# Kernel optimization log

Measured on AMD Instinct MI355X. Metric: run time of the kernel, lower is better.

## Reference

```python
import jax, jax.numpy as jnp
import numpy as np

V, E, H2, K = 30000, 256, 256, 13  # vocab, embed dim, per-direction hidden, num tags
B, T = 64, 512


def setup_inputs() -> dict:
    key = jax.random.key(0)
    ks = jax.random.split(key, 12)
    s = 0.1
    return {
        "x": jax.random.randint(ks[0], (B, T), 0, V, dtype=jnp.int32),
        "emb": jax.random.normal(ks[1], (V, E), dtype=jnp.float32) * s,
        "w_ih_f": jax.random.normal(ks[2], (4 * H2, E), dtype=jnp.float32) * s,
        "w_hh_f": jax.random.normal(ks[3], (4 * H2, H2), dtype=jnp.float32) * s,
        "b_ih_f": jnp.zeros((4 * H2,), jnp.float32),
        "b_hh_f": jnp.zeros((4 * H2,), jnp.float32),
        "w_ih_b": jax.random.normal(ks[4], (4 * H2, E), dtype=jnp.float32) * s,
        "w_hh_b": jax.random.normal(ks[5], (4 * H2, H2), dtype=jnp.float32) * s,
        "b_ih_b": jnp.zeros((4 * H2,), jnp.float32),
        "b_hh_b": jnp.zeros((4 * H2,), jnp.float32),
        "w_out": jax.random.normal(ks[6], (K, 2 * H2), dtype=jnp.float32) * s,
        "b_out": jnp.zeros((K,), jnp.float32),
        "start_trans": jax.random.normal(ks[7], (K,), dtype=jnp.float32) * s,
        "end_trans": jax.random.normal(ks[8], (K,), dtype=jnp.float32) * s,
        "trans": jax.random.normal(ks[9], (K, K), dtype=jnp.float32) * s,
    }


def _lstm_dir(xg, w_hh, reverse):
    # xg: [T, B, 4H] precomputed input-side gate pre-activations (PyTorch i|f|g|o order)
    Bsz, H = xg.shape[1], w_hh.shape[1]

    def step(carry, g_in):
        h, c = carry
        g = g_in + h @ w_hh.T
        i, f, gg, o = jnp.split(g, 4, axis=-1)
        c = jax.nn.sigmoid(f) * c + jax.nn.sigmoid(i) * jnp.tanh(gg)
        h = jax.nn.sigmoid(o) * jnp.tanh(c)
        return (h, c), h

    init = (jnp.zeros((Bsz, H), xg.dtype), jnp.zeros((Bsz, H), xg.dtype))
    _, hs = jax.lax.scan(step, init, xg, reverse=reverse)
    return hs  # [T, B, H]


def reference(x, emb, w_ih_f, w_hh_f, b_ih_f, b_hh_f, w_ih_b, w_hh_b, b_ih_b, b_hh_b,
              w_out, b_out, start_trans, end_trans, trans):
    e = emb[x].transpose(1, 0, 2)                     # [T, B, E] time-major
    xg_f = e @ w_ih_f.T + (b_ih_f + b_hh_f)           # [T, B, 4H] (fold both biases)
    xg_b = e @ w_ih_b.T + (b_ih_b + b_hh_b)
    h_f = _lstm_dir(xg_f, w_hh_f, reverse=False)
    h_b = _lstm_dir(xg_b, w_hh_b, reverse=True)
    h = jnp.concatenate([h_f, h_b], axis=-1)          # [T, B, 2H]; dropout = identity (eval)
    emissions = h @ w_out.T + b_out                   # [T, B, K]

    # CRF Viterbi decode (torchcrf semantics, full mask)
    score = start_trans + emissions[0]                # [B, K]

    def vstep(score, emit_t):
        s = score[:, :, None] + trans[None] + emit_t[:, None, :]  # [B, K_prev, K_next]
        return s.max(axis=1), s.argmax(axis=1)

    score, bps = jax.lax.scan(vstep, score, emissions[1:])        # bps: [T-1, B, K]
    score = score + end_trans
    best_last = jnp.argmax(score, axis=-1)            # [B]
    best_score = jnp.max(score, axis=-1)              # [B]

    def btstep(tag, bp_t):
        prev = jnp.take_along_axis(bp_t, tag[:, None], axis=1)[:, 0]
        return prev, prev

    _, path_head = jax.lax.scan(btstep, best_last, bps, reverse=True)  # [T-1, B]
    path = jnp.concatenate([path_head, best_last[None]], axis=0).T     # [B, T]
    return path, best_score
```

## Files before the change

### kernel.cpp

```cpp
#include <hip/hip_runtime.h>
#include <stdint.h>
#include <stddef.h>

#define T_LEN  512
#define BATCH  64
#define NTAG   13
#define CT     64
#define NCHUNK 8

__device__ __forceinline__ float sigm(float x) { return 1.0f / (1.0f + expf(-x)); }

__global__ __launch_bounds__(256) void xg_gemm(
    const int* __restrict__ x, const float* __restrict__ emb,
    const float* __restrict__ w_ih_f, const float* __restrict__ w_ih_b,
    const float* __restrict__ b_ih_f, const float* __restrict__ b_hh_f,
    const float* __restrict__ b_ih_b, const float* __restrict__ b_hh_b,
    float* __restrict__ xg_ws, int chunk)
{
    const int tid = threadIdx.x;
    const int mt = blockIdx.x;
    const int nt = blockIdx.y;
    const int d  = blockIdx.z;
    const int tbase = (d == 0 ? chunk : (NCHUNK - 1 - chunk)) * CT;
    const float* W  = (d == 0) ? w_ih_f : w_ih_b;
    const float* bi = (d == 0) ? b_ih_f : b_ih_b;
    const float* bh = (d == 0) ? b_hh_f : b_hh_b;

    __shared__ __align__(16) float Wl[16][132];
    __shared__ __align__(16) float El[16][132];
    __shared__ int tok[128];

    if (tid < 128) {
        int col = nt * 128 + tid;
        tok[tid] = x[(col & 63) * T_LEN + tbase + (col >> 6)];
    }
    __syncthreads();

    const int r  = tid >> 1;
    const int c8 = (tid & 1) * 8;
    const int tm = tid >> 4;
    const int tn = tid & 15;

    float acc[8][8];
#pragma unroll
    for (int i = 0; i < 8; i++)
#pragma unroll
        for (int jz = 0; jz < 8; jz++) acc[i][jz] = 0.0f;

    const float* wrow = &W[(size_t)(mt * 128 + r) * 256];
    const float* erow = &emb[(size_t)tok[r] * 256];

    for (int kb = 0; kb < 256; kb += 16) {
        float4 w0 = *(const float4*)&wrow[kb + c8];
        float4 w1 = *(const float4*)&wrow[kb + c8 + 4];
        float4 e0 = *(const float4*)&erow[kb + c8];
        float4 e1 = *(const float4*)&erow[kb + c8 + 4];
        __syncthreads();
        Wl[c8+0][r] = w0.x; Wl[c8+1][r] = w0.y; Wl[c8+2][r] = w0.z; Wl[c8+3][r] = w0.w;
        Wl[c8+4][r] = w1.x; Wl[c8+5][r] = w1.y; Wl[c8+6][r] = w1.z; Wl[c8+7][r] = w1.w;
        El[c8+0][r] = e0.x; El[c8+1][r] = e0.y; El[c8+2][r] = e0.z; El[c8+3][r] = e0.w;
        El[c8+4][r] = e1.x; El[c8+5][r] = e1.y; El[c8+6][r] = e1.z; El[c8+7][r] = e1.w;
        __syncthreads();
#pragma unroll
        for (int kk = 0; kk < 16; kk++) {
            float a[8], b[8];
            *(float4*)&a[0] = *(const float4*)&Wl[kk][tm*8];
            *(float4*)&a[4] = *(const float4*)&Wl[kk][tm*8+4];
            *(float4*)&b[0] = *(const float4*)&El[kk][tn*8];
            *(float4*)&b[4] = *(const float4*)&El[kk][tn*8+4];
#pragma unroll
            for (int i = 0; i < 8; i++)
#pragma unroll
                for (int jz = 0; jz < 8; jz++)
                    acc[i][jz] += a[i] * b[jz];
        }
    }

    const int colbase = nt * 128 + tn * 8;
    const int j  = colbase >> 6;
    const int b0 = colbase & 63;
#pragma unroll
    for (int gi = 0; gi < 8; gi++) {
        int g = mt * 128 + tm * 8 + gi;
        float bias = bi[g] + bh[g];
        float* dst = &xg_ws[(((size_t)(d * CT + j) * 1024 + g) << 6) + b0];
        float4 v0 = make_float4(acc[gi][0]+bias, acc[gi][1]+bias, acc[gi][2]+bias, acc[gi][3]+bias);
        float4 v1 = make_float4(acc[gi][4]+bias, acc[gi][5]+bias, acc[gi][6]+bias, acc[gi][7]+bias);
        *(float4*)dst       = v0;
        *(float4*)(dst + 4) = v1;
    }
}

__global__ __launch_bounds__(256) void lstm_chunk(
    const float* __restrict__ xg_ws,
    const float* __restrict__ w_hh_f, const float* __restrict__ w_hh_b,
    float* h_ex, float* c_state, float* h_all, int* flags, int chunk)
{
    const int tid = threadIdx.x;
    const int bid = blockIdx.x;
    const int dg    = bid & 7;
    const int slice = bid >> 3;
    const int dir = dg & 1;
    const int grp = dg >> 1;
    const int h_base = slice * 8;
    const int sbase  = grp * 16;

    __shared__ __align__(16) float w_lds[32][260];
    __shared__ __align__(16) float h_lds[16][260];
    __shared__ __align__(16) float red[4][32][20];
    __shared__ float gatebuf[32][17];

    const float* W = dir ? w_hh_b : w_hh_f;
    for (int idx = tid; idx < 32 * 256; idx += 256) {
        int rr = idx >> 8, jj = idx & 255;
        w_lds[rr][jj] = W[(size_t)((rr >> 3) * 256 + h_base + (rr & 7)) * 256 + jj];
    }

    const int s_g  = tid & 15;
    const int ih_g = tid >> 4;
    float c_val = 0.0f;
    if (tid < 128)
        c_val = c_state[(size_t)(dir * 64 + sbase + s_g) * 256 + h_base + ih_g];

    {
        const int s = tid >> 4, tn = tid & 15;
        const float* src = &h_ex[((size_t)dg * 16 + s) * 256];
#pragma unroll
        for (int i = 0; i < 16; i++)
            h_lds[s][tn + 16 * i] =
                __hip_atomic_load(&src[tn + 16 * i], __ATOMIC_RELAXED, __HIP_MEMORY_SCOPE_AGENT);
    }
    __syncthreads();

    const int kc   = tid >> 5;
    const int tile = tid & 31;
    const int gt = tile >> 2;
    const int st = tile & 3;
    const float* wr[4] = { &w_lds[gt][0], &w_lds[8+gt][0], &w_lds[16+gt][0], &w_lds[24+gt][0] };
    const float* hr[4] = { &h_lds[st][0], &h_lds[4+st][0], &h_lds[8+st][0],  &h_lds[12+st][0] };

    float xg0 = 0.f, xg1 = 0.f, xg2 = 0.f, xg3 = 0.f;
    {
        const int jslot0 = dir ? (CT - 1) : 0;
        if (tid < 128) {
            const float* xp = &xg_ws[(((size_t)(dir * CT + jslot0) * 1024) + h_base + ih_g) * 64 + sbase + s_g];
            xg0 = xp[0];
            xg1 = xp[1 * 256 * 64];
            xg2 = xp[2 * 256 * 64];
            xg3 = xp[3 * 256 * 64];
        }
    }

#pragma unroll 1
    for (int tl = 0; tl < CT; tl++) {
        const int jslot = dir ? (CT - 1 - tl) : tl;
        const int t = (dir ? (NCHUNK - 1 - chunk) : chunk) * CT + jslot;
        const int sc = chunk * CT + tl + 1;
        const int par = sc & 1;

        float acc[4][4];
#pragma unroll
        for (int gi = 0; gi < 4; gi++)
#pragma unroll
            for (int si = 0; si < 4; si++) acc[gi][si] = 0.0f;

        const int j0 = kc * 32;
#pragma unroll
        for (int m = 0; m < 8; m++) {
            const int jj = j0 + m * 4;
            float4 w4[4], h4[4];
#pragma unroll
            for (int i = 0; i < 4; i++) w4[i] = *(const float4*)(wr[i] + jj);
#pragma unroll
            for (int i = 0; i < 4; i++) h4[i] = *(const float4*)(hr[i] + jj);
#pragma unroll
            for (int gi = 0; gi < 4; gi++)
#pragma unroll
                for (int si = 0; si < 4; si++)
                    acc[gi][si] += w4[gi].x*h4[si].x + w4[gi].y*h4[si].y
                                 + w4[gi].z*h4[si].z + w4[gi].w*h4[si].w;
        }

        if (kc >= 4) {
#pragma unroll
            for (int gi = 0; gi < 4; gi++)
                *(float4*)&red[kc-4][tile][gi*4] =
                    make_float4(acc[gi][0], acc[gi][1], acc[gi][2], acc[gi][3]);
        }
        __syncthreads();
        if (kc < 4) {
#pragma unroll
            for (int gi = 0; gi < 4; gi++) {
                float4 v = *(const float4*)&red[kc][tile][gi*4];
                acc[gi][0] += v.x; acc[gi][1] += v.y; acc[gi][2] += v.z; acc[gi][3] += v.w;
            }
        }
        __syncthreads();
        if (kc >= 1 && kc < 4) {
#pragma unroll
            for (int gi = 0; gi < 4; gi++)
                *(float4*)&red[kc-1][tile][gi*4] =
                    make_float4(acc[gi][0], acc[gi][1], acc[gi][2], acc[gi][3]);
        }
        __syncthreads();
        if (kc == 0) {
#pragma unroll
            for (int p = 0; p < 3; p++)
#pragma unroll
                for (int gi = 0; gi < 4; gi++) {
                    float4 v = *(const float4*)&red[p][tile][gi*4];
                    acc[gi][0] += v.x; acc[gi][1] += v.y; acc[gi][2] += v.z; acc[gi][3] += v.w;
                }
#pragma unroll
            for (int gi = 0; gi < 4; gi++)
#pragma unroll
                for (int si = 0; si < 4; si++)
                    gatebuf[8*gi + gt][4*si + st] = acc[gi][si];
        }
        __syncthreads();

        float hv = 0.0f;
        if (tid < 128) {
            float gI = gatebuf[ih_g     ][s_g] + xg0;
            float gF = gatebuf[8  + ih_g][s_g] + xg1;
            float gG = gatebuf[16 + ih_g][s_g] + xg2;
            float gO = gatebuf[24 + ih_g][s_g] + xg3;
            c_val = sigm(gF) * c_val + sigm(gI) * tanhf(gG);
            hv = sigm(gO) * tanhf(c_val);
            __hip_atomic_store(&h_ex[(((size_t)par * 8 + dg) * 16 + s_g) * 256 + h_base + ih_g],
                               hv, __ATOMIC_RELAXED, __HIP_MEMORY_SCOPE_AGENT);
        }
        __syncthreads();

        if (tid == 0)
            __hip_atomic_store(&flags[dg * 32 + slice], sc, __ATOMIC_RELAXED, __HIP_MEMORY_SCOPE_AGENT);

        if (tid < 128) {
            h_all[((size_t)t * 64 + sbase + s_g) * 512 + dir * 256 + h_base + ih_g] = hv;
            if (tl + 1 < CT) {
                const int jn = dir ? (jslot - 1) : (jslot + 1);
                const float* xp = &xg_ws[(((size_t)(dir * CT + jn) * 1024) + h_base + ih_g) * 64 + sbase + s_g];
                xg0 = xp[0];
                xg1 = xp[1 * 256 * 64];
                xg2 = xp[2 * 256 * 64];
                xg3 = xp[3 * 256 * 64];
            }
        }

        if (tid < 64) {
            const int* fp = &flags[dg * 32 + (tid & 31)];
            int guard = 0;
            int v = __hip_atomic_load(fp, __ATOMIC_RELAXED, __HIP_MEMORY_SCOPE_AGENT);
            while (__ballot(v < sc) != 0ull) {
                __builtin_amdgcn_s_sleep(4);
                v = __hip_atomic_load(fp, __ATOMIC_RELAXED, __HIP_MEMORY_SCOPE_AGENT);
                if (++guard > (1 << 20)) break;
            }
        }
        __syncthreads();

        {
            const int s = tid >> 4, tn = tid & 15;
            const float* src = &h_ex[(((size_t)par * 8 + dg) * 16 + s) * 256];
#pragma unroll
            for (int i = 0; i < 16; i++)
                h_lds[s][tn + 16 * i] =
                    __hip_atomic_load(&src[tn + 16 * i], __ATOMIC_RELAXED, __HIP_MEMORY_SCOPE_AGENT);
        }
        __syncthreads();
    }

    if (tid < 128)
        c_state[(size_t)(dir * 64 + sbase + s_g) * 256 + h_base + ih_g] = c_val;
}

__global__ __launch_bounds__(256) void emis_kernel(
    const float* __restrict__ h_all, const float* __restrict__ w_out,
    const float* __restrict__ b_out, float* __restrict__ emis)
{
    const int row = blockIdx.x * 16 + (threadIdx.x >> 4);
    const int k   = threadIdx.x & 15;
    const float* hr = &h_all[(size_t)row * 512];
    const float* wr = &w_out[(size_t)(k < NTAG ? k : 0) * 512];
    float acc = 0.0f;
#pragma unroll 8
    for (int e = 0; e < 512; e += 4) {
        float4 h4 = *(const float4*)&hr[e];
        float4 w4 = *(const float4*)&wr[e];
        acc += h4.x*w4.x + h4.y*w4.y + h4.z*w4.z + h4.w*w4.w;
    }
    if (k < NTAG) emis[(size_t)row * NTAG + k] = acc + b_out[k];
}

__global__ __launch_bounds__(64) void viterbi_kernel(
    const float* __restrict__ emis, const float* __restrict__ start_trans,
    const float* __restrict__ end_trans, const float* __restrict__ trans,
    float* __restrict__ out)
{
    const int b = blockIdx.x;
    const int k = threadIdx.x;
    __shared__ float em[T_LEN * NTAG];
    __shared__ unsigned char bp[T_LEN][16];

    for (int t = k; t < T_LEN; t += 64) {
        const float* src = &emis[((size_t)t * 64 + b) * NTAG];
#pragma unroll
        for (int kk = 0; kk < NTAG; kk++)
            em[t * NTAG + kk] = src[kk];
    }
    __syncthreads();

    float tc[NTAG];
#pragma unroll
    for (int kp = 0; kp < NTAG; kp++)
        tc[kp] = (k < NTAG) ? trans[kp * NTAG + k] : 0.0f;

    float score = (k < NTAG) ? (start_trans[k] + em[k]) : -3.0e38f;

    for (int t = 1; t < T_LEN; t++) {
        float best = -3.0e38f;
        int bi = 0;
#pragma unroll
        for (int kp = 0; kp < NTAG; kp++) {
            float v = __shfl(score, kp) + tc[kp];
            if (v > best) { best = v; bi = kp; }
        }
        if (k < NTAG) {
            score = best + em[t * NTAG + k];
            bp[t][k] = (unsigned char)bi;
        }
    }
    if (k < NTAG) score += end_trans[k];
    else score = -3.0e38f;
    __syncthreads();

    float bs = -3.0e38f;
    int tag = 0;
#pragma unroll
    for (int kk = 0; kk < NTAG; kk++) {
        float v = __shfl(score, kk);
        if (v > bs) { bs = v; tag = kk; }
    }
    if (k == 0) {
        out[32768 + b] = bs;
        int tg = tag;
        out[b * T_LEN + (T_LEN - 1)] = (float)tg;
        for (int t = T_LEN - 1; t >= 1; t--) {
            tg = bp[t][tg];
            out[b * T_LEN + t - 1] = (float)tg;
        }
    }
}

extern "C" void kernel_launch(void* const* d_in, const int* in_sizes, int n_in,
                              void* d_out, int out_size, void* d_ws, size_t ws_size,
                              hipStream_t stream)
{
    (void)in_sizes; (void)n_in; (void)out_size; (void)ws_size;
    const int*   x    = (const int*)  d_in[0];
    const float* emb  = (const float*)d_in[1];
    const float* wihf = (const float*)d_in[2];
    const float* whhf = (const float*)d_in[3];
    const float* bihf = (const float*)d_in[4];
    const float* bhhf = (const float*)d_in[5];
    const float* wihb = (const float*)d_in[6];
    const float* whhb = (const float*)d_in[7];
    const float* bihb = (const float*)d_in[8];
    const float* bhhb = (const float*)d_in[9];
    const float* wout = (const float*)d_in[10];
    const float* bout = (const float*)d_in[11];
    const float* stt  = (const float*)d_in[12];
    const float* ent  = (const float*)d_in[13];
    const float* trn  = (const float*)d_in[14];
    float* out = (float*)d_out;

    char* ws = (char*)d_ws;
    size_t off = 0;
    float* xg_ws = (float*)(ws + off); off += (size_t)2 * CT * 1024 * 64 * 4;
    float* h_all = (float*)(ws + off); off += (size_t)T_LEN * 64 * 512 * 4;
    float* h_ex  = (float*)(ws + off); off += (size_t)2 * 8 * 16 * 256 * 4;
    float* c_st  = (float*)(ws + off); off += (size_t)2 * 64 * 256 * 4;
    float* emis  = (float*)(ws + off); off += (size_t)T_LEN * 64 * NTAG * 4;
    int*   flags = (int*)  (ws + off); off += 8 * 32 * 4;

    hipMemsetAsync(h_ex,  0, (size_t)2 * 8 * 16 * 256 * 4, stream);
    hipMemsetAsync(c_st,  0, (size_t)2 * 64 * 256 * 4, stream);
    hipMemsetAsync(flags, 0, 8 * 32 * 4, stream);

    for (int c = 0; c < NCHUNK; c++) {
        xg_gemm<<<dim3(8, 32, 2), 256, 0, stream>>>(x, emb, wihf, wihb,
                                                    bihf, bhhf, bihb, bhhb, xg_ws, c);
        lstm_chunk<<<256, 256, 0, stream>>>(xg_ws, whhf, whhb, h_ex, c_st, h_all, flags, c);
    }
    emis_kernel<<<2048, 256, 0, stream>>>(h_all, wout, bout, emis);
    viterbi_kernel<<<64, 64, 0, stream>>>(emis, stt, ent, trn, out);
}
```

Measured before the change: 3.833 ms.

## Halve LSTM recurrence grid by giving each block 16 hidden units

Each persistent recurrence block now owns 16 hidden units (64 gate rows) instead of 8, so the grid drops from 256 to 128 blocks. All 256 threads take part in the gate nonlinearity, and each group barrier waits on 16 flags instead of 32. The intent is to cut the cost of cross-block synchronisation per timestep and to use otherwise idle threads. In exchange each block does twice the FMA work per step, holds more registers and LDS, and the spin-wait now sleeps only after a few polls.

```diff
diff --git a/kernel.cpp b/kernel.cpp
--- a/kernel.cpp
+++ b/kernel.cpp
@@ -101,26 +101,26 @@
     const int dg    = bid & 7;
     const int slice = bid >> 3;
     const int dir = dg & 1;
-    const int grp = dg >> 1;
-    const int h_base = slice * 8;
-    const int sbase  = grp * 16;
-
-    __shared__ __align__(16) float w_lds[32][260];
+    const int sg  = dg >> 1;
+    const int h_base = slice * 16;
+    const int sbase  = sg * 16;
+
+    __shared__ __align__(16) float w_lds[64][260];
     __shared__ __align__(16) float h_lds[16][260];
-    __shared__ __align__(16) float red[4][32][20];
-    __shared__ float gatebuf[32][17];
+    __shared__ __align__(16) float red[4][32][36];
+    __shared__ float gatebuf[64][17];
 
     const float* W = dir ? w_hh_b : w_hh_f;
-    for (int idx = tid; idx < 32 * 256; idx += 256) {
-        int rr = idx >> 8, jj = idx & 255;
-        w_lds[rr][jj] = W[(size_t)((rr >> 3) * 256 + h_base + (rr & 7)) * 256 + jj];
+    for (int idx = tid; idx < 4096; idx += 256) {
+        int rr = idx >> 6;
+        int c4 = (idx & 63) << 2;
+        int row = (rr >> 4) * 256 + h_base + (rr & 15);
+        *(float4*)&w_lds[rr][c4] = *(const float4*)&W[(size_t)row * 256 + c4];
     }
 
     const int s_g  = tid & 15;
     const int ih_g = tid >> 4;
-    float c_val = 0.0f;
-    if (tid < 128)
-        c_val = c_state[(size_t)(dir * 64 + sbase + s_g) * 256 + h_base + ih_g];
+    float c_val = c_state[(size_t)(dir * 64 + sbase + s_g) * 256 + h_base + ih_g];
 
     {
         const int s = tid >> 4, tn = tid & 15;
@@ -134,21 +134,23 @@
 
     const int kc   = tid >> 5;
     const int tile = tid & 31;
-    const int gt = tile >> 2;
-    const int st = tile & 3;
-    const float* wr[4] = { &w_lds[gt][0], &w_lds[8+gt][0], &w_lds[16+gt][0], &w_lds[24+gt][0] };
-    const float* hr[4] = { &h_lds[st][0], &h_lds[4+st][0], &h_lds[8+st][0],  &h_lds[12+st][0] };
+    const int rowt = tile >> 2;
+    const int st   = tile & 3;
+    const float* wrp[8];
+#pragma unroll
+    for (int i = 0; i < 8; i++) wrp[i] = &w_lds[rowt + i * 8][0];
+    const float* hrp[4];
+#pragma unroll
+    for (int i = 0; i < 4; i++) hrp[i] = &h_lds[st + i * 4][0];
 
     float xg0 = 0.f, xg1 = 0.f, xg2 = 0.f, xg3 = 0.f;
     {
         const int jslot0 = dir ? (CT - 1) : 0;
-        if (tid < 128) {
-            const float* xp = &xg_ws[(((size_t)(dir * CT + jslot0) * 1024) + h_base + ih_g) * 64 + sbase + s_g];
-            xg0 = xp[0];
-            xg1 = xp[1 * 256 * 64];
-            xg2 = xp[2 * 256 * 64];
-            xg3 = xp[3 * 256 * 64];
-        }
+        const float* xp = &xg_ws[(((size_t)(dir * CT + jslot0) * 1024) + h_base + ih_g) * 64 + sbase + s_g];
+        xg0 = xp[0];
+        xg1 = xp[1 * 256 * 64];
+        xg2 = xp[2 * 256 * 64];
+        xg3 = xp[3 * 256 * 64];
     }
 
 #pragma unroll 1
@@ -158,103 +160,98 @@
         const int sc = chunk * CT + tl + 1;
         const int par = sc & 1;
 
-        float acc[4][4];
-#pragma unroll
-        for (int gi = 0; gi < 4; gi++)
-#pragma unroll
-            for (int si = 0; si < 4; si++) acc[gi][si] = 0.0f;
+        float acc[8][4];
+#pragma unroll
+        for (int ri = 0; ri < 8; ri++)
+#pragma unroll
+            for (int si = 0; si < 4; si++) acc[ri][si] = 0.0f;
 
         const int j0 = kc * 32;
 #pragma unroll
         for (int m = 0; m < 8; m++) {
             const int jj = j0 + m * 4;
-            float4 w4[4], h4[4];
-#pragma unroll
-            for (int i = 0; i < 4; i++) w4[i] = *(const float4*)(wr[i] + jj);
-#pragma unroll
-            for (int i = 0; i < 4; i++) h4[i] = *(const float4*)(hr[i] + jj);
-#pragma unroll
-            for (int gi = 0; gi < 4; gi++)
+            float4 h4[4];
+#pragma unroll
+            for (int i = 0; i < 4; i++) h4[i] = *(const float4*)(hrp[i] + jj);
+#pragma unroll
+            for (int ri = 0; ri < 8; ri++) {
+                float4 w4 = *(const float4*)(wrp[ri] + jj);
 #pragma unroll
                 for (int si = 0; si < 4; si++)
-                    acc[gi][si] += w4[gi].x*h4[si].x + w4[gi].y*h4[si].y
-                                 + w4[gi].z*h4[si].z + w4[gi].w*h4[si].w;
+                    acc[ri][si] += w4.x*h4[si].x + w4.y*h4[si].y
+                                 + w4.z*h4[si].z + w4.w*h4[si].w;
+            }
         }
 
         if (kc >= 4) {
 #pragma unroll
-            for (int gi = 0; gi < 4; gi++)
-                *(float4*)&red[kc-4][tile][gi*4] =
-                    make_float4(acc[gi][0], acc[gi][1], acc[gi][2], acc[gi][3]);
+            for (int ri = 0; ri < 8; ri++)
+                *(float4*)&red[kc-4][tile][ri*4] =
+                    make_float4(acc[ri][0], acc[ri][1], acc[ri][2], acc[ri][3]);
         }
         __syncthreads();
         if (kc < 4) {
 #pragma unroll
-            for (int gi = 0; gi < 4; gi++) {
-                float4 v = *(const float4*)&red[kc][tile][gi*4];
-                acc[gi][0] += v.x; acc[gi][1] += v.y; acc[gi][2] += v.z; acc[gi][3] += v.w;
+            for (int ri = 0; ri < 8; ri++) {
+                float4 v = *(const float4*)&red[kc][tile][ri*4];
+                acc[ri][0] += v.x; acc[ri][1] += v.y; acc[ri][2] += v.z; acc[ri][3] += v.w;
             }
         }
         __syncthreads();
         if (kc >= 1 && kc < 4) {
 #pragma unroll
-            for (int gi = 0; gi < 4; gi++)
-                *(float4*)&red[kc-1][tile][gi*4] =
-                    make_float4(acc[gi][0], acc[gi][1], acc[gi][2], acc[gi][3]);
+            for (int ri = 0; ri < 8; ri++)
+                *(float4*)&red[kc-1][tile][ri*4] =
+                    make_float4(acc[ri][0], acc[ri][1], acc[ri][2], acc[ri][3]);
         }
         __syncthreads();
         if (kc == 0) {
 #pragma unroll
             for (int p = 0; p < 3; p++)
 #pragma unroll
-                for (int gi = 0; gi < 4; gi++) {
-                    float4 v = *(const float4*)&red[p][tile][gi*4];
-                    acc[gi][0] += v.x; acc[gi][1] += v.y; acc[gi][2] += v.z; acc[gi][3] += v.w;
+                for (int ri = 0; ri < 8; ri++) {
+                    float4 v = *(const float4*)&red[p][tile][ri*4];
+                    acc[ri][0] += v.x; acc[ri][1] += v.y; acc[ri][2] += v.z; acc[ri][3] += v.w;
                 }
 #pragma unroll
-            for (int gi = 0; gi < 4; gi++)
+            for (int ri = 0; ri < 8; ri++)
 #pragma unroll
                 for (int si = 0; si < 4; si++)
-                    gatebuf[8*gi + gt][4*si + st] = acc[gi][si];
-        }
-        __syncthreads();
-
-        float hv = 0.0f;
-        if (tid < 128) {
-            float gI = gatebuf[ih_g     ][s_g] + xg0;
-            float gF = gatebuf[8  + ih_g][s_g] + xg1;
-            float gG = gatebuf[16 + ih_g][s_g] + xg2;
-            float gO = gatebuf[24 + ih_g][s_g] + xg3;
-            c_val = sigm(gF) * c_val + sigm(gI) * tanhf(gG);
-            hv = sigm(gO) * tanhf(c_val);
-            __hip_atomic_store(&h_ex[(((size_t)par * 8 + dg) * 16 + s_g) * 256 + h_base + ih_g],
-                               hv, __ATOMIC_RELAXED, __HIP_MEMORY_SCOPE_AGENT);
-        }
+                    gatebuf[rowt + ri*8][st + si*4] = acc[ri][si];
+        }
+        __syncthreads();
+
+        float gI = gatebuf[     ih_g][s_g] + xg0;
+        float gF = gatebuf[16 + ih_g][s_g] + xg1;
+        float gG = gatebuf[32 + ih_g][s_g] + xg2;
+        float gO = gatebuf[48 + ih_g][s_g] + xg3;
+        c_val = sigm(gF) * c_val + sigm(gI) * tanhf(gG);
+        float hv = sigm(gO) * tanhf(c_val);
+        __hip_atomic_store(&h_ex[(((size_t)par * 8 + dg) * 16 + s_g) * 256 + h_base + ih_g],
+                           hv, __ATOMIC_RELAXED, __HIP_MEMORY_SCOPE_AGENT);
         __syncthreads();
 
         if (tid == 0)
-            __hip_atomic_store(&flags[dg * 32 + slice], sc, __ATOMIC_RELAXED, __HIP_MEMORY_SCOPE_AGENT);
-
-        if (tid < 128) {
-            h_all[((size_t)t * 64 + sbase + s_g) * 512 + dir * 256 + h_base + ih_g] = hv;
-            if (tl + 1 < CT) {
-                const int jn = dir ? (jslot - 1) : (jslot + 1);
-                const float* xp = &xg_ws[(((size_t)(dir * CT + jn) * 1024) + h_base + ih_g) * 64 + sbase + s_g];
-                xg0 = xp[0];
-                xg1 = xp[1 * 256 * 64];
-                xg2 = xp[2 * 256 * 64];
-                xg3 = xp[3 * 256 * 64];
-            }
+            __hip_atomic_store(&flags[dg * 16 + slice], sc, __ATOMIC_RELAXED, __HIP_MEMORY_SCOPE_AGENT);
+
+        h_all[((size_t)t * 64 + sbase + s_g) * 512 + dir * 256 + h_base + ih_g] = hv;
+        if (tl + 1 < CT) {
+            const int jn = dir ? (jslot - 1) : (jslot + 1);
+            const float* xp = &xg_ws[(((size_t)(dir * CT + jn) * 1024) + h_base + ih_g) * 64 + sbase + s_g];
+            xg0 = xp[0];
+            xg1 = xp[1 * 256 * 64];
+            xg2 = xp[2 * 256 * 64];
+            xg3 = xp[3 * 256 * 64];
         }
 
         if (tid < 64) {
-            const int* fp = &flags[dg * 32 + (tid & 31)];
-            int guard = 0;
+            const int* fp = &flags[dg * 16 + (tid & 15)];
+            int spins = 0;
             int v = __hip_atomic_load(fp, __ATOMIC_RELAXED, __HIP_MEMORY_SCOPE_AGENT);
             while (__ballot(v < sc) != 0ull) {
-                __builtin_amdgcn_s_sleep(4);
+                if (++spins > 4) __builtin_amdgcn_s_sleep(2);
                 v = __hip_atomic_load(fp, __ATOMIC_RELAXED, __HIP_MEMORY_SCOPE_AGENT);
-                if (++guard > (1 << 20)) break;
+                if (spins > (1 << 20)) break;
             }
         }
         __syncthreads();
@@ -270,8 +267,7 @@
         __syncthreads();
     }
 
-    if (tid < 128)
-        c_state[(size_t)(dir * 64 + sbase + s_g) * 256 + h_base + ih_g] = c_val;
+    c_state[(size_t)(dir * 64 + sbase + s_g) * 256 + h_base + ih_g] = c_val;
 }
 
 __global__ __launch_bounds__(256) void emis_kernel(
@@ -381,16 +377,16 @@
     float* h_ex  = (float*)(ws + off); off += (size_t)2 * 8 * 16 * 256 * 4;
     float* c_st  = (float*)(ws + off); off += (size_t)2 * 64 * 256 * 4;
     float* emis  = (float*)(ws + off); off += (size_t)T_LEN * 64 * NTAG * 4;
-    int*   flags = (int*)  (ws + off); off += 8 * 32 * 4;
+    int*   flags = (int*)  (ws + off); off += 8 * 16 * 4;
 
     hipMemsetAsync(h_ex,  0, (size_t)2 * 8 * 16 * 256 * 4, stream);
     hipMemsetAsync(c_st,  0, (size_t)2 * 64 * 256 * 4, stream);
-    hipMemsetAsync(flags, 0, 8 * 32 * 4, stream);
+    hipMemsetAsync(flags, 0, 8 * 16 * 4, stream);
 
     for (int c = 0; c < NCHUNK; c++) {
         xg_gemm<<<dim3(8, 32, 2), 256, 0, stream>>>(x, emb, wihf, wihb,
                                                     bihf, bhhf, bihb, bhhb, xg_ws, c);
-        lstm_chunk<<<256, 256, 0, stream>>>(xg_ws, whhf, whhb, h_ex, c_st, h_all, flags, c);
+        lstm_chunk<<<128, 256, 0, stream>>>(xg_ws, whhf, whhb, h_ex, c_st, h_all, flags, c);
     }
     emis_kernel<<<2048, 256, 0, stream>>>(h_all, wout, bout, emis);
     viterbi_kernel<<<64, 64, 0, stream>>>(emis, stt, ent, trn, out);
```

New measurement: 4.583 ms. +19.6%, slower.
